# Optimization experiments

Hardware: AMD Instinct MI355X
Metric: run time of the kernel (lower is better)

The kernel has to match this reference:

```python
import jax, jax.numpy as jnp
import numpy as np

DT = 0.02
N_STEPS = 50
BATCH = 131072
DIM = 3


def setup_inputs() -> dict:
    key = jax.random.key(0)
    ks = jax.random.split(key, 10)

    def lin(k, fan_in, fan_out):
        return jax.random.normal(k, (fan_in, fan_out), jnp.float32) / jnp.sqrt(jnp.float32(fan_in))

    return {
        "y0": jax.random.normal(ks[0], (DIM,), jnp.float32),
        "Y0": jnp.zeros((1, 1), jnp.float32),
        "qW1": lin(ks[1], DIM + 1, 64), "qb1": jnp.zeros((64,), jnp.float32),
        "qW2": lin(ks[2], 64, 64),      "qb2": jnp.zeros((64,), jnp.float32),
        "qW3": lin(ks[3], 64, 1),       "qb3": jnp.zeros((1,), jnp.float32),
        "zW1": lin(ks[4], DIM + 1, 64), "zb1": jnp.zeros((64,), jnp.float32),
        "zW2": lin(ks[5], 64, 64),      "zb2": jnp.zeros((64,), jnp.float32),
        "zW3": lin(ks[6], 64, 3),       "zb3": jnp.zeros((3,), jnp.float32),
        # pre-drawn standard normals; scaled by sqrt(dt) inside reference
        "dW": jax.random.normal(ks[7], (N_STEPS, BATCH, 3), jnp.float32),
    }


def _mlp(x, W1, b1, W2, b2, W3, b3):
    h = jax.nn.relu(x @ W1 + b1)
    h = jax.nn.relu(h @ W2 + b2)
    return h @ W3 + b3


def reference(y0, Y0, qW1, qb1, qW2, qb2, qW3, qb3,
              zW1, zb1, zW2, zb2, zW3, zb3, dW):
    n_steps, B, _ = dW.shape
    dt = jnp.float32(DT)
    sqrt_dt = jnp.sqrt(dt)
    eye3 = jnp.eye(DIM, dtype=y0.dtype)

    y_init = jnp.broadcast_to(y0[None, :], (B, DIM))
    Y_init = jnp.broadcast_to(Y0, (B, 1))
    ts = jnp.arange(n_steps, dtype=y0.dtype) * dt

    def step(carry, xs):
        y, Y, res = carry
        t_scalar, dWn = xs
        t = jnp.full((B, 1), t_scalar, dtype=y.dtype)
        x = jnp.concatenate([t, y], axis=1)                      # [B, dim+1]
        z = _mlp(x, zW1, zb1, zW2, zb2, zW3, zb3)                # [B, 3]
        q = _mlp(x, qW1, qb1, qW2, qb2, qW3, qb3)                # [B, 1]
        f = 0.5 * q ** 2                                         # generator
        dWs = dWn * sqrt_dt                                      # [B, 3]
        mu = -y + q                                              # drift, [B, dim]
        sigma = (0.2 + 0.1 * jnp.tanh(y))[:, :, None] * eye3     # [B, dim, 3]
        diffusion = jnp.einsum('bij,bj->bi', sigma, dWs)
        y_next = y + mu * dt + diffusion
        Y_next = Y - f * dt + jnp.sum(z * dWs, axis=1, keepdims=True)
        # residual = detach(Y_next) - (Y - f*dt + (z*dW).sum()) == 0 identically
        residual = jax.lax.stop_gradient(Y_next - Y_next)
        res = res + jnp.mean(residual ** 2)
        return (y_next, Y_next, res), None

    (y, Y, total_res), _ = jax.lax.scan(
        step, (y_init, Y_init, jnp.float32(0.0)), (ts, dW))
    terminal = jnp.sum(y ** 2, axis=1, keepdims=True)            # terminal cost
    return jnp.mean((Y - terminal) ** 2) + total_res
```

## Files before the change

kernel.cpp:

```cpp
#include <hip/hip_runtime.h>
#include <math.h>

#define N_STEPS 50
#define DT 0.02f

typedef __attribute__((ext_vector_type(8))) short    bf16x8;
typedef __attribute__((ext_vector_type(4))) float    f32x4;
typedef __attribute__((ext_vector_type(4))) unsigned u32x4;

__device__ inline unsigned f2bf(float f) {
    unsigned u = __builtin_bit_cast(unsigned, f);
    return ((u + 0x7FFFu + ((u >> 16) & 1u)) >> 16);
}
__device__ inline unsigned pk2(float lo, float hi) {
    return (f2bf(lo) & 0xFFFFu) | (f2bf(hi) << 16);
}
__device__ inline unsigned cvtpk(float lo, float hi) {
    unsigned r;
    asm("v_cvt_pk_bf16_f32 %0, %1, %2" : "=v"(r) : "v"(lo), "v"(hi));
    return r;
}
__device__ inline bf16x8 mk8(unsigned a, unsigned b, unsigned cc, unsigned d) {
    u32x4 t; t.x = a; t.y = b; t.z = cc; t.w = d;
    return __builtin_bit_cast(bf16x8, t);
}
__device__ inline float fast_tanh(float x) {
    float e, r;
    asm("v_exp_f32 %0, %1" : "=v"(e) : "v"(x * 2.8853900817779268f));
    asm("v_rcp_f32 %0, %1" : "=v"(r) : "v"(e + 1.0f));
    return fmaf(-2.0f, r, 1.0f);
}

__device__ inline float red4(const float pv[4], int g) {
    float r4[4];
#pragma unroll
    for (int t4 = 0; t4 < 4; ++t4) {
        float v = pv[t4];
        v += __shfl_xor(v, 16, 64);
        v += __shfl_xor(v, 32, 64);
        r4[t4] = v;
    }
    float pick = r4[0];
    pick = (g == 1) ? r4[1] : pick;
    pick = (g == 2) ? r4[2] : pick;
    pick = (g == 3) ? r4[3] : pick;
    return pick;
}

__global__ __launch_bounds__(64, 2) void bsde_kernel(
    const float* __restrict__ y0v, const float* __restrict__ Y0v,
    const float* __restrict__ qW1, const float* __restrict__ qb1,
    const float* __restrict__ qW2, const float* __restrict__ qb2,
    const float* __restrict__ qW3, const float* __restrict__ qb3,
    const float* __restrict__ zW1, const float* __restrict__ zb1,
    const float* __restrict__ zW2, const float* __restrict__ zb2,
    const float* __restrict__ zW3, const float* __restrict__ zb3,
    const float* __restrict__ dW,
    float* __restrict__ out, int B)
{
    const int lane = threadIdx.x;
    const int c    = lane & 15;
    const int g    = lane >> 4;
    const int p    = blockIdx.x * 64 + lane;

    __shared__ unsigned short ex[64 * 128];
    __shared__ __align__(16) float w3c[4][64];

    w3c[0][lane] = zW3[3 * lane + 0];
    w3c[1][lane] = zW3[3 * lane + 1];
    w3c[2][lane] = zW3[3 * lane + 2];
    w3c[3][lane] = qW3[lane];

    bf16x8 w1f[8];
#pragma unroll
    for (int mt = 0; mt < 8; ++mt) {
        const float* W1 = (mt < 4) ? zW1 : qW1;
        const float* b1 = (mt < 4) ? zb1 : qb1;
        const int h = 16 * (mt & 3) + c;
        unsigned d0 = 0, d1 = 0, d2 = 0;
        if (g == 0) {
            d0 = pk2(W1[0 * 64 + h], W1[1 * 64 + h]);
            d1 = pk2(W1[2 * 64 + h], W1[3 * 64 + h]);
            d2 = f2bf(b1[h]) & 0xFFFFu;
        }
        w1f[mt] = mk8(d0, d1, d2, 0);
    }

    bf16x8 w2f[8][2];
#pragma unroll
    for (int mt = 0; mt < 8; ++mt) {
        const float* W2 = (mt < 4) ? zW2 : qW2;
        const int h = 16 * (mt & 3) + c;
#pragma unroll
        for (int kt = 0; kt < 2; ++kt) {
            const int k0 = 32 * kt + 8 * g;
            w2f[mt][kt] = mk8(
                pk2(W2[(k0 + 0) * 64 + h], W2[(k0 + 1) * 64 + h]),
                pk2(W2[(k0 + 2) * 64 + h], W2[(k0 + 3) * 64 + h]),
                pk2(W2[(k0 + 4) * 64 + h], W2[(k0 + 5) * 64 + h]),
                pk2(W2[(k0 + 6) * 64 + h], W2[(k0 + 7) * 64 + h]));
        }
    }

    f32x4 b2v[8];
#pragma unroll
    for (int mt = 0; mt < 8; ++mt) {
        const float* b2 = (mt < 4) ? zb2 : qb2;
#pragma unroll
        for (int r = 0; r < 4; ++r)
            b2v[mt][r] = b2[16 * (mt & 3) + 4 * g + r];
    }

    const float zb3_0 = zb3[0], zb3_1 = zb3[1], zb3_2 = zb3[2];
    const float qb3_0 = qb3[0];

    __syncthreads();

    char* exn = (char*)ex;
    const int sw = (c & 7) << 4;
    const unsigned jp2c = (g == 0) ? 0x3F80u : 0u;

    const float sqrt_dt = sqrtf(DT);
    float y0 = y0v[0], y1 = y0v[1], y2 = y0v[2];
    float Y  = Y0v[0];

    for (int n = 0; n < N_STEPS; ++n) {
        const float t = (float)n * DT;

        const size_t idx = ((size_t)n * (size_t)B + (size_t)p) * 3;
        const float dr0 = dW[idx + 0];
        const float dr1 = dW[idx + 1];
        const float dr2 = dW[idx + 2];

#pragma unroll
        for (int t4 = 0; t4 < 4; ++t4) {
            const int src = 16 * t4 + c;
            const float s0 = __shfl(y0, src, 64);
            const float s1 = __shfl(y1, src, 64);
            const float s2 = __shfl(y2, src, 64);
            const unsigned a = cvtpk(t,  s0);
            const unsigned b = cvtpk(s1, s2);
            const bf16x8 xf = mk8((g == 0) ? a : 0u, (g == 0) ? b : 0u, jp2c, 0u);
#pragma unroll
            for (int mt = 0; mt < 8; ++mt) {
                f32x4 c1 = __builtin_amdgcn_mfma_f32_16x16x32_bf16(
                    w1f[mt], xf, (f32x4){0.f, 0.f, 0.f, 0.f}, 0, 0, 0);
                const unsigned lo = cvtpk(fmaxf(c1[0], 0.f), fmaxf(c1[1], 0.f));
                const unsigned hi = cvtpk(fmaxf(c1[2], 0.f), fmaxf(c1[3], 0.f));
                const int off = (((16 * t4 + c) * 256) + (mt >> 2) * 128
                                 + 32 * (mt & 3) + 8 * g) ^ sw;
                *(unsigned long long*)(exn + off) =
                    ((unsigned long long)hi << 32) | (unsigned long long)lo;
            }
        }

        float pz0[4] = {0.f, 0.f, 0.f, 0.f};
        float pz1[4] = {0.f, 0.f, 0.f, 0.f};
        float pz2[4] = {0.f, 0.f, 0.f, 0.f};
        float pq [4] = {0.f, 0.f, 0.f, 0.f};
#pragma unroll
        for (int mt = 0; mt < 8; ++mt) {
            const int hb = 16 * (mt & 3) + 4 * g;
            f32x4 wz0, wz1, wz2, wq;
            if (mt < 4) {
                wz0 = *(const f32x4*)&w3c[0][hb];
                wz1 = *(const f32x4*)&w3c[1][hb];
                wz2 = *(const f32x4*)&w3c[2][hb];
            } else {
                wq  = *(const f32x4*)&w3c[3][hb];
            }
#pragma unroll
            for (int t4 = 0; t4 < 4; ++t4) {
                const int rb = ((16 * t4 + c) * 256) + (mt >> 2) * 128 + 16 * g;
                const bf16x8 hf0 = *(const bf16x8*)(exn + ((rb +  0) ^ sw));
                const bf16x8 hf1 = *(const bf16x8*)(exn + ((rb + 64) ^ sw));
                f32x4 acc = __builtin_amdgcn_mfma_f32_16x16x32_bf16(
                    w2f[mt][0], hf0, b2v[mt], 0, 0, 0);
                acc = __builtin_amdgcn_mfma_f32_16x16x32_bf16(
                    w2f[mt][1], hf1, acc, 0, 0, 0);
#pragma unroll
                for (int r = 0; r < 4; ++r) {
                    const float h = fmaxf(acc[r], 0.f);
                    if (mt < 4) {
                        pz0[t4] = fmaf(h, wz0[r], pz0[t4]);
                        pz1[t4] = fmaf(h, wz1[r], pz1[t4]);
                        pz2[t4] = fmaf(h, wz2[r], pz2[t4]);
                    } else {
                        pq[t4]  = fmaf(h, wq[r],  pq[t4]);
                    }
                }
            }
        }

        const float oz0 = red4(pz0, g) + zb3_0;
        const float oz1 = red4(pz1, g) + zb3_1;
        const float oz2 = red4(pz2, g) + zb3_2;
        const float qq  = red4(pq,  g) + qb3_0;

        const float dw0 = dr0 * sqrt_dt;
        const float dw1 = dr1 * sqrt_dt;
        const float dw2 = dr2 * sqrt_dt;

        const float f = 0.5f * qq * qq;
        Y = Y - f * DT + (oz0 * dw0 + oz1 * dw1 + oz2 * dw2);

        const float s0 = 0.2f + 0.1f * fast_tanh(y0);
        const float s1 = 0.2f + 0.1f * fast_tanh(y1);
        const float s2 = 0.2f + 0.1f * fast_tanh(y2);
        y0 = y0 + (qq - y0) * DT + s0 * dw0;
        y1 = y1 + (qq - y1) * DT + s1 * dw1;
        y2 = y2 + (qq - y2) * DT + s2 * dw2;
    }

    const float term = y0 * y0 + y1 * y1 + y2 * y2;
    const float d    = Y - term;
    float val = d * d;
#pragma unroll
    for (int off = 32; off > 0; off >>= 1)
        val += __shfl_down(val, off, 64);
    if (lane == 0)
        atomicAdd(out, val * (1.0f / (float)B));
}

extern "C" void kernel_launch(void* const* d_in, const int* in_sizes, int n_in,
                              void* d_out, int out_size, void* d_ws, size_t ws_size,
                              hipStream_t stream) {
    const float* y0  = (const float*)d_in[0];
    const float* Y0  = (const float*)d_in[1];
    const float* qW1 = (const float*)d_in[2];
    const float* qb1 = (const float*)d_in[3];
    const float* qW2 = (const float*)d_in[4];
    const float* qb2 = (const float*)d_in[5];
    const float* qW3 = (const float*)d_in[6];
    const float* qb3 = (const float*)d_in[7];
    const float* zW1 = (const float*)d_in[8];
    const float* zb1 = (const float*)d_in[9];
    const float* zW2 = (const float*)d_in[10];
    const float* zb2 = (const float*)d_in[11];
    const float* zW3 = (const float*)d_in[12];
    const float* zb3 = (const float*)d_in[13];
    const float* dW  = (const float*)d_in[14];

    const int B = in_sizes[14] / (N_STEPS * 3);
    float* out = (float*)d_out;

    hipMemsetAsync(out, 0, sizeof(float), stream);

    const int threads = 64;
    const int blocks  = B / 64;
    bsde_kernel<<<blocks, threads, 0, stream>>>(
        y0, Y0, qW1, qb1, qW2, qb2, qW3, qb3,
        zW1, zb1, zW2, zb2, zW3, zb3, dW, out, B);
}
```

Before: 400.6 us.

## Process 32 samples per wavefront and raise occupancy to four waves

Each 64-lane block now handles 32 batch paths instead of 64. Upper lane groups duplicate the lower ones, and the hidden-layer tile loops shrink from four to two. The LDS exchange buffer is halved, the grid is doubled, and launch bounds allow four blocks per CU, so the MFMA chain is spread over more resident waves for better latency hiding. In exchange, the elementwise state update and the dW loads are done redundantly in half the lanes, and the cross-lane reduction is rewritten for two tiles.

Measured after the change: 874.6 us. 2.18x slower.

```diff
diff --git a/kernel.cpp b/kernel.cpp
--- a/kernel.cpp
+++ b/kernel.cpp
@@ -31,23 +31,15 @@
     return fmaf(-2.0f, r, 1.0f);
 }
 
-__device__ inline float red4(const float pv[4], int g) {
-    float r4[4];
-#pragma unroll
-    for (int t4 = 0; t4 < 4; ++t4) {
-        float v = pv[t4];
-        v += __shfl_xor(v, 16, 64);
-        v += __shfl_xor(v, 32, 64);
-        r4[t4] = v;
-    }
-    float pick = r4[0];
-    pick = (g == 1) ? r4[1] : pick;
-    pick = (g == 2) ? r4[2] : pick;
-    pick = (g == 3) ? r4[3] : pick;
-    return pick;
-}
-
-__global__ __launch_bounds__(64, 2) void bsde_kernel(
+__device__ inline float red2(const float pv[2], int gp) {
+    float x = gp ? pv[1] : pv[0];
+    float o = gp ? pv[0] : pv[1];
+    x += __shfl_xor(o, 16, 64);
+    x += __shfl_xor(x, 32, 64);
+    return x;
+}
+
+__global__ __launch_bounds__(64, 4) void bsde_kernel(
     const float* __restrict__ y0v, const float* __restrict__ Y0v,
     const float* __restrict__ qW1, const float* __restrict__ qb1,
     const float* __restrict__ qW2, const float* __restrict__ qb2,
@@ -61,9 +53,10 @@
     const int lane = threadIdx.x;
     const int c    = lane & 15;
     const int g    = lane >> 4;
-    const int p    = blockIdx.x * 64 + lane;
-
-    __shared__ unsigned short ex[64 * 128];
+    const int gp   = g & 1;
+    const int p    = blockIdx.x * 32 + 16 * gp + c;
+
+    __shared__ unsigned short ex[32 * 128];
     __shared__ __align__(16) float w3c[4][64];
 
     w3c[0][lane] = zW3[3 * lane + 0];
@@ -133,7 +126,7 @@
         const float dr2 = dW[idx + 2];
 
 #pragma unroll
-        for (int t4 = 0; t4 < 4; ++t4) {
+        for (int t4 = 0; t4 < 2; ++t4) {
             const int src = 16 * t4 + c;
             const float s0 = __shfl(y0, src, 64);
             const float s1 = __shfl(y1, src, 64);
@@ -154,10 +147,10 @@
             }
         }
 
-        float pz0[4] = {0.f, 0.f, 0.f, 0.f};
-        float pz1[4] = {0.f, 0.f, 0.f, 0.f};
-        float pz2[4] = {0.f, 0.f, 0.f, 0.f};
-        float pq [4] = {0.f, 0.f, 0.f, 0.f};
+        float pz0[2] = {0.f, 0.f};
+        float pz1[2] = {0.f, 0.f};
+        float pz2[2] = {0.f, 0.f};
+        float pq [2] = {0.f, 0.f};
 #pragma unroll
         for (int mt = 0; mt < 8; ++mt) {
             const int hb = 16 * (mt & 3) + 4 * g;
@@ -170,7 +163,7 @@
                 wq  = *(const f32x4*)&w3c[3][hb];
             }
 #pragma unroll
-            for (int t4 = 0; t4 < 4; ++t4) {
+            for (int t4 = 0; t4 < 2; ++t4) {
                 const int rb = ((16 * t4 + c) * 256) + (mt >> 2) * 128 + 16 * g;
                 const bf16x8 hf0 = *(const bf16x8*)(exn + ((rb +  0) ^ sw));
                 const bf16x8 hf1 = *(const bf16x8*)(exn + ((rb + 64) ^ sw));
@@ -192,10 +185,10 @@
             }
         }
 
-        const float oz0 = red4(pz0, g) + zb3_0;
-        const float oz1 = red4(pz1, g) + zb3_1;
-        const float oz2 = red4(pz2, g) + zb3_2;
-        const float qq  = red4(pq,  g) + qb3_0;
+        const float oz0 = red2(pz0, gp) + zb3_0;
+        const float oz1 = red2(pz1, gp) + zb3_1;
+        const float oz2 = red2(pz2, gp) + zb3_2;
+        const float qq  = red2(pq,  gp) + qb3_0;
 
         const float dw0 = dr0 * sqrt_dt;
         const float dw1 = dr1 * sqrt_dt;
@@ -214,7 +207,7 @@
 
     const float term = y0 * y0 + y1 * y1 + y2 * y2;
     const float d    = Y - term;
-    float val = d * d;
+    float val = (g < 2) ? d * d : 0.0f;
 #pragma unroll
     for (int off = 32; off > 0; off >>= 1)
         val += __shfl_down(val, off, 64);
@@ -247,7 +240,7 @@
     hipMemsetAsync(out, 0, sizeof(float), stream);
 
     const int threads = 64;
-    const int blocks  = B / 64;
+    const int blocks  = B / 32;
     bsde_kernel<<<blocks, threads, 0, stream>>>(
         y0, Y0, qW1, qb1, qW2, qb2, qW3, qb3,
         zW1, zb1, zW2, zb2, zW3, zb3, dW, out, B);
```
